# Optimization experiments

Measured on AMD Instinct MI355X. Metric: run time of the kernel, lower is better.

The kernel has to match this reference:

```python
import jax, jax.numpy as jnp
import numpy as np

V, H, B, T_ENC, S, T_DEC, G = 18000, 400, 16, 256, 30, 8, 3


def setup_inputs() -> dict:
    key = jax.random.key(0)
    ks = jax.random.split(key, 16)
    def n(k, shape, s=0.1):
        return jax.random.normal(k, shape, jnp.float32) * s
    return {
        'story': jax.random.randint(ks[0], (B, T_ENC), 0, V, dtype=jnp.int32),
        'target_batches': jax.random.randint(ks[1], (B, S, T_DEC), 0, V, dtype=jnp.int32),
        'emb': n(ks[2], (V, H)),
        'enc_Wih_f': n(ks[3], (3 * H, H)), 'enc_Whh_f': n(ks[4], (3 * H, H)),
        'enc_bih_f': jnp.zeros((3 * H,), jnp.float32), 'enc_bhh_f': jnp.zeros((3 * H,), jnp.float32),
        'enc_Wih_b': n(ks[5], (3 * H, H)), 'enc_Whh_b': n(ks[6], (3 * H, H)),
        'enc_bih_b': jnp.zeros((3 * H,), jnp.float32), 'enc_bhh_b': jnp.zeros((3 * H,), jnp.float32),
        'dec_Wih': n(ks[7], (3 * H, H)), 'dec_Whh': n(ks[8], (3 * H, H)),
        'dec_bih': jnp.zeros((3 * H,), jnp.float32), 'dec_bhh': jnp.zeros((3 * H,), jnp.float32),
        'W_ratio': n(ks[9], (1, 3 * H)), 'b_ratio': jnp.zeros((1,), jnp.float32),
        'W_gate': n(ks[10], (G, H)), 'b_gate': jnp.zeros((G,), jnp.float32),
        'slot_emb': n(ks[11], (S, H)),
    }


def _gru_step(h, x, Wih, Whh, bih, bhh):
    # PyTorch GRU gate order: r, z, n
    gi = x @ Wih.T + bih
    gh = h @ Whh.T + bhh
    ir, iz, ig = jnp.split(gi, 3, axis=-1)
    hr, hz, hg = jnp.split(gh, 3, axis=-1)
    r = jax.nn.sigmoid(ir + hr)
    z = jax.nn.sigmoid(iz + hz)
    g = jnp.tanh(ig + r * hg)
    return (1.0 - z) * g + z * h


def _run_gru(xs, h0, Wih, Whh, bih, bhh):
    def step(h, x):
        h2 = _gru_step(h, x, Wih, Whh, bih, bhh)
        return h2, h2
    hT, out = jax.lax.scan(step, h0, xs)
    return out, hT


def reference(story, target_batches, emb,
              enc_Wih_f, enc_Whh_f, enc_bih_f, enc_bhh_f,
              enc_Wih_b, enc_Whh_b, enc_bih_b, enc_bhh_b,
              dec_Wih, dec_Whh, dec_bih, dec_bhh,
              W_ratio, b_ratio, W_gate, b_gate, slot_emb):
    # ---- EncoderRNN (bidirectional 1-layer GRU; dropout=0 / eval mode) ----
    x = emb[story.T]                       # (T_enc, B, H)
    h0 = jnp.zeros((B, H), x.dtype)
    out_f, h_f = _run_gru(x, h0, enc_Wih_f, enc_Whh_f, enc_bih_f, enc_bhh_f)
    out_b_rev, h_b = _run_gru(x[::-1], h0, enc_Wih_b, enc_Whh_b, enc_bih_b, enc_bhh_b)
    out_b = out_b_rev[::-1]
    enc_out = jnp.transpose(out_f + out_b, (1, 0, 2))   # (B, T_enc, H) = fwd+bwd halves summed
    enc_hidden = h_f + h_b                               # (B, H)     = hidden[0] + hidden[1]

    # ---- Generator decode loop ----
    SB = S * B
    dec_in0 = jnp.broadcast_to(slot_emb[:, None, :], (S, B, H)).reshape(SB, H)
    h = jnp.tile(enc_hidden, (S, 1))                     # (SB, H)
    enc_tiled = jnp.tile(enc_out, (S, 1, 1))             # (SB, T_enc, H)
    story_tiled = jnp.tile(story, (S, 1))                # (SB, T_enc)
    rows = jnp.arange(SB)[:, None]
    # teacher-forcing tokens per step, slot-major flatten to (T_dec, SB)
    tf_tokens = jnp.transpose(target_batches, (2, 1, 0)).reshape(T_DEC, SB)

    def step(carry, tok):
        h, dec_in = carry
        h2 = _gru_step(h, dec_in, dec_Wih, dec_Whh, dec_bih, dec_bhh)  # dec_state == new hidden
        scores = jnp.einsum('nd,ntd->nt', h2, enc_tiled)               # attend (all lens == T_enc)
        prob = jax.nn.softmax(scores, axis=1)
        context = jnp.einsum('nt,ntd->nd', prob, enc_tiled)
        gate = context @ W_gate.T + b_gate                              # (SB, G)
        p_vocab = jax.nn.softmax(h2 @ emb.T, axis=1)                    # (SB, V)
        p_gen = jnp.concatenate([h2, context, dec_in], axis=-1)         # (SB, 3H)
        sw = jax.nn.sigmoid(p_gen @ W_ratio.T + b_ratio)                # (SB, 1)
        ptr = jnp.zeros((SB, V), prob.dtype).at[rows, story_tiled].add(prob)  # scatter_add copy dist
        final = (1.0 - sw) * ptr + sw * p_vocab
        dec_in_next = emb[tok]                                          # teacher forcing
        return (h2, dec_in_next), (final, gate)

    _, (finals, gates) = jax.lax.scan(step, (h, dec_in0), tf_tokens)
    all_pointer_outputs = finals.reshape(T_DEC, S, B, V).transpose(1, 2, 0, 3)  # (S, B, T_dec, V)
    all_gate_outputs = gates[0].reshape(S, B, G)                                 # gate from step 0
    return all_pointer_outputs, all_gate_outputs
```

## Files before the change

kernel.cpp:

```cpp
#include <hip/hip_runtime.h>
#include <cstdint>
#include <cstddef>

#define VV 18000
#define HH 400
#define H3 1200
#define H3P 1280
#define KP 416
#define BB 16
#define TE 256
#define SS 30
#define TDN 8
#define GGN 3
#define SBN 480
#define NROW_ENC 4096
#define VP 18048
#define MP_DEC 512

#define EBLK 25

typedef __bf16 bf16;
typedef __attribute__((ext_vector_type(8))) __bf16 bf16x8;
typedef __attribute__((ext_vector_type(4))) float f32x4;
typedef __attribute__((ext_vector_type(4))) unsigned int u32x4;

static __device__ __forceinline__ float sigf(float x) {
    return 1.0f / (1.0f + __expf(-x));
}

__global__ __launch_bounds__(256) void gemm_bt(const bf16* __restrict__ A,
                                               const bf16* __restrict__ B,
                                               float* __restrict__ C,
                                               int M, int N, int K) {
    __shared__ __align__(16) bf16 sA[128 * 32];
    __shared__ __align__(16) bf16 sB[128 * 32];
    const int tid = threadIdx.x;
    const int lane = tid & 63;
    const int wave = tid >> 6;
    const int wm = wave >> 1, wn = wave & 1;
    const int m0 = blockIdx.x * 128, n0 = blockIdx.y * 128;
    f32x4 acc[4][4] = {};
    const int c0 = tid, c1 = tid + 256;
    const int r0 = c0 >> 2, q0 = (c0 & 3) * 8;
    const int r1 = c1 >> 2, q1 = (c1 & 3) * 8;
    const int ar = lane & 15, ak = (lane >> 4) * 8;
    const int nk = K >> 5;
    for (int kt = 0; kt < nk; ++kt) {
        const int kb = kt * 32;
        uint4 a0 = *(const uint4*)(A + (size_t)(m0 + r0) * K + kb + q0);
        uint4 a1 = *(const uint4*)(A + (size_t)(m0 + r1) * K + kb + q1);
        uint4 b0 = *(const uint4*)(B + (size_t)(n0 + r0) * K + kb + q0);
        uint4 b1 = *(const uint4*)(B + (size_t)(n0 + r1) * K + kb + q1);
        __syncthreads();
        *(uint4*)(sA + r0 * 32 + q0) = a0;
        *(uint4*)(sA + r1 * 32 + q1) = a1;
        *(uint4*)(sB + r0 * 32 + q0) = b0;
        *(uint4*)(sB + r1 * 32 + q1) = b1;
        __syncthreads();
        bf16x8 af[4], bg[4];
#pragma unroll
        for (int i = 0; i < 4; ++i)
            af[i] = *(const bf16x8*)(sA + (wm * 64 + i * 16 + ar) * 32 + ak);
#pragma unroll
        for (int j = 0; j < 4; ++j)
            bg[j] = *(const bf16x8*)(sB + (wn * 64 + j * 16 + ar) * 32 + ak);
#pragma unroll
        for (int i = 0; i < 4; ++i)
#pragma unroll
            for (int j = 0; j < 4; ++j)
                acc[i][j] = __builtin_amdgcn_mfma_f32_16x16x32_bf16(af[i], bg[j], acc[i][j], 0, 0, 0);
    }
    const int cr = (lane >> 4) * 4, cc = lane & 15;
#pragma unroll
    for (int i = 0; i < 4; ++i)
#pragma unroll
        for (int j = 0; j < 4; ++j)
#pragma unroll
            for (int q = 0; q < 4; ++q) {
                int row = m0 + wm * 64 + i * 16 + cr + q;
                int col = n0 + wn * 64 + j * 16 + cc;
                C[(size_t)row * N + col] = acc[i][j][q];
            }
}

__global__ void prep_pad_bf16(const float* __restrict__ src, bf16* __restrict__ dst,
                              int rows_real, int cols_real, int rows_pad, int cols_pad) {
    int idx = blockIdx.x * blockDim.x + threadIdx.x;
    int total = rows_pad * cols_pad;
    if (idx >= total) return;
    int r = idx / cols_pad, c = idx % cols_pad;
    float v = (r < rows_real && c < cols_real) ? src[(size_t)r * cols_real + c] : 0.f;
    dst[idx] = (bf16)v;
}

__global__ void prep_aenc(const int* __restrict__ story, const float* __restrict__ emb,
                          bf16* __restrict__ dst) {
    int idx = blockIdx.x * blockDim.x + threadIdx.x;
    if (idx >= NROW_ENC * KP) return;
    int m = idx / KP, k = idx % KP;
    int t = m >> 4, b = m & 15;
    float v = 0.f;
    if (k < HH) {
        int tok = story[b * TE + t];
        v = emb[(size_t)tok * HH + k];
    }
    dst[idx] = (bf16)v;
}

__global__ void prep_decx(const int* __restrict__ target, const float* __restrict__ emb,
                          const float* __restrict__ slot, float* __restrict__ xf,
                          bf16* __restrict__ xb) {
    int idx = blockIdx.x * blockDim.x + threadIdx.x;
    if (idx >= TDN * SBN * KP) return;
    int k = idx % KP;
    int nn = idx / KP;
    int n = nn % SBN;
    int td = nn / SBN;
    int s = n >> 4, b = n & 15;
    float v = 0.f;
    if (k < HH) {
        if (td == 0) v = slot[s * HH + k];
        else {
            int tok = target[(b * SS + s) * TDN + (td - 1)];
            v = emb[(size_t)tok * HH + k];
        }
        xf[((size_t)td * SBN + n) * HH + k] = v;
    }
    xb[idx] = (bf16)v;
}

__global__ void zero_bf16k(bf16* dst, int total) {
    int idx = blockIdx.x * blockDim.x + threadIdx.x;
    if (idx < total) dst[idx] = (bf16)0.f;
}

__global__ __launch_bounds__(256) void enc_rnn10(
    const float* __restrict__ gi_f, const float* __restrict__ gi_b,
    const float* __restrict__ whh_f, const float* __restrict__ whh_b,
    const float* __restrict__ bih_f, const float* __restrict__ bhh_f,
    const float* __restrict__ bih_b, const float* __restrict__ bhh_b,
    float* __restrict__ hist_f, float* __restrict__ hist_b,
    unsigned int* __restrict__ hbuf_f, unsigned int* __restrict__ hbuf_b,
    unsigned int* __restrict__ flags) {
    const int dir = blockIdx.x & 1;
    const int blk = blockIdx.x >> 1;
    const int j0 = blk * 16;
    const float* gi  = dir ? gi_b : gi_f;
    const float* whh = dir ? whh_b : whh_f;
    const float* bih = dir ? bih_b : bih_f;
    const float* bhh = dir ? bhh_b : bhh_f;
    float* hist = dir ? hist_b : hist_f;
    unsigned int* hbuf = dir ? hbuf_b : hbuf_f;

    __shared__ float GHL[3 * 256];

    const int tid = threadIdx.x;
    const int wv = tid >> 6, lane = tid & 63;

    const int ub = tid >> 4, ucol = tid & 15;
    const int uj = j0 + ucol;
    const float bihr = bih[uj], bihz = bih[HH + uj], bihg = bih[2 * HH + uj];
    const float bhhr = bhh[uj], bhhz = bhh[HH + uj], bhhg = bhh[2 * HH + uj];

    const int kk0 = (lane >> 4) * 8;
    bf16x8 Bf[13];
    if (wv < 3) {
        const int brow = wv * HH + j0 + (lane & 15);
#pragma unroll
        for (int ks = 0; ks < 13; ++ks) {
            bf16x8 v;
#pragma unroll
            for (int e = 0; e < 8; ++e) {
                int k = kk0 + ks * 32 + e;
                v[e] = (k < HH) ? (bf16)whh[(size_t)brow * HH + k] : (bf16)0.f;
            }
            Bf[ks] = v;
        }
    }

    union UV { unsigned int d[4]; bf16x8 v; };

    float hp = 0.f;

    for (int s = 0; s < TE; ++s) {
        const int tt = dir ? (TE - 1 - s) : s;
        const float* gir = gi + ((size_t)tt * BB + ub) * H3P;
        float gi0 = gir[uj];
        float gi1 = gir[HH + uj];
        float gi2 = gir[2 * HH + uj];

        f32x4 acc0 = {}, acc1 = {};
        if (s > 0) {
            if (wv == 0) {
                const unsigned int* fl = flags + ((size_t)dir * TE + (s - 1)) * 32;
                while (true) {
                    unsigned f = 1u;
                    if (lane < EBLK)
                        asm volatile("global_load_dword %0, %1, off sc0 sc1"
                                     : "=v"(f) : "v"(fl + lane));
                    asm volatile("s_waitcnt vmcnt(0)" ::: "memory");
                    if (__all((int)(f != 0u))) break;
                }
            }
            __syncthreads();
            if (wv < 3) {
                const int ttp = dir ? (tt + 1) : (tt - 1);
                const unsigned int* hrow =
                    hbuf + ((size_t)ttp * BB + (lane & 15)) * KP + kk0;
                u32x4 ua[13], ubv[13];
#pragma unroll
                for (int ks = 0; ks < 13; ++ks) {
                    asm volatile("global_load_dwordx4 %0, %1, off offset:%c2 sc0 sc1"
                                 : "=v"(ua[ks]) : "v"(hrow), "n"(ks * 128));
                    asm volatile("global_load_dwordx4 %0, %1, off offset:%c2 sc0 sc1"
                                 : "=v"(ubv[ks]) : "v"(hrow), "n"(ks * 128 + 16));
                }
                asm volatile("s_waitcnt vmcnt(0)" ::: "memory");
                __builtin_amdgcn_sched_barrier(0);
#pragma unroll
                for (int ks = 0; ks < 13; ++ks) {
                    u32x4 a = ua[ks], b = ubv[ks];
                    UV ah, al;
                    ah.d[0] = (a.x & 0xffffu) | (a.y << 16);
                    ah.d[1] = (a.z & 0xffffu) | (a.w << 16);
                    ah.d[2] = (b.x & 0xffffu) | (b.y << 16);
                    ah.d[3] = (b.z & 0xffffu) | (b.w << 16);
                    al.d[0] = (a.x >> 16) | (a.y & 0xffff0000u);
                    al.d[1] = (a.z >> 16) | (a.w & 0xffff0000u);
                    al.d[2] = (b.x >> 16) | (b.y & 0xffff0000u);
                    al.d[3] = (b.z >> 16) | (b.w & 0xffff0000u);
                    acc0 = __builtin_amdgcn_mfma_f32_16x16x32_bf16(ah.v, Bf[ks], acc0, 0, 0, 0);
                    acc1 = __builtin_amdgcn_mfma_f32_16x16x32_bf16(al.v, Bf[ks], acc1, 0, 0, 0);
                }
            }
        }
        if (wv < 3) {
            f32x4 at = acc0 + acc1;
            const int cb0 = wv * 256 + ((lane >> 4) * 4) * 16 + (lane & 15);
            GHL[cb0]      = at[0];
            GHL[cb0 + 16] = at[1];
            GHL[cb0 + 32] = at[2];
            GHL[cb0 + 48] = at[3];
        }
        __syncthreads();

        float ghr = GHL[tid];
        float ghz = GHL[256 + tid];
        float ghg = GHL[512 + tid];
        float r = sigf(gi0 + bihr + ghr + bhhr);
        float z = sigf(gi1 + bihz + ghz + bhhz);
        float g = tanhf(gi2 + bihg + r * (ghg + bhhg));
        float hn = (1.f - z) * g + z * hp;
        hp = hn;
        hist[((size_t)tt * BB + ub) * HH + uj] = hn;
        bf16 hi = (bf16)hn;
        bf16 lo = (bf16)(hn - (float)hi);
        unsigned int pk = (unsigned int)__builtin_bit_cast(unsigned short, hi)
                        | ((unsigned int)__builtin_bit_cast(unsigned short, lo) << 16);
        unsigned int* hw = hbuf + ((size_t)tt * BB + ub) * KP + uj;
        asm volatile("global_store_dword %0, %1, off sc0 sc1" :: "v"(hw), "v"(pk) : "memory");

        asm volatile("s_waitcnt vmcnt(0)" ::: "memory");
        __syncthreads();
        if (tid == 0) {
            unsigned int one = 1u;
            unsigned int* fw = flags + ((size_t)dir * TE + s) * 32 + blk;
            asm volatile("global_store_dword %0, %1, off sc0 sc1" :: "v"(fw), "v"(one) : "memory");
        }
    }
}

__global__ void combine_enc(const float* __restrict__ hf, const float* __restrict__ hb,
                            float* __restrict__ enc_out) {
    int idx = blockIdx.x * blockDim.x + threadIdx.x;
    if (idx >= BB * TE * HH) return;
    int hcol = idx % HH;
    int t = (idx / HH) % TE;
    int b = idx / (HH * TE);
    size_t src = ((size_t)t * BB + b) * HH + hcol;
    enc_out[idx] = hf[src] + hb[src];
}

__global__ void init_hdec2(const float* __restrict__ hf, const float* __restrict__ hb,
                           float* __restrict__ hdec, bf16* __restrict__ h2b) {
    int idx = blockIdx.x * blockDim.x + threadIdx.x;
    if (idx >= SBN * HH) return;
    int hcol = idx % HH;
    int n = idx / HH;
    int b = n & 15;
    float v = hf[((size_t)(TE - 1) * BB + b) * HH + hcol] + hb[((size_t)b) * HH + hcol];
    hdec[idx] = v;
    h2b[(size_t)n * KP + hcol] = (bf16)v;
}

__global__ void gru_dec2(const float* __restrict__ gi, const float* __restrict__ gh,
                         const float* __restrict__ bih, const float* __restrict__ bhh,
                         const float* __restrict__ hprev, float* __restrict__ hnew,
                         bf16* __restrict__ h2b) {
    int idx = blockIdx.x * blockDim.x + threadIdx.x;
    if (idx >= SBN * HH) return;
    int n = idx / HH, j = idx % HH;
    const float* gir = gi + (size_t)n * H3P;
    const float* ghr = gh + (size_t)n * H3P;
    float r = sigf(gir[j] + bih[j] + ghr[j] + bhh[j]);
    float z = sigf(gir[HH + j] + bih[HH + j] + ghr[HH + j] + bhh[HH + j]);
    float g = tanhf(gir[2 * HH + j] + bih[2 * HH + j] + r * (ghr[2 * HH + j] + bhh[2 * HH + j]));
    float hn = (1.f - z) * g + z * hprev[idx];
    hnew[idx] = hn;
    h2b[(size_t)n * KP + j] = (bf16)hn;
}

__global__ __launch_bounds__(256) void attn2(const float* __restrict__ h2,
                                             const float* __restrict__ enc,
                                             const float* __restrict__ dx,
                                             const float* __restrict__ Wr, const float* __restrict__ br,
                                             const float* __restrict__ Wg, const float* __restrict__ bg,
                                             float* __restrict__ prob,
                                             float* __restrict__ sw, float* __restrict__ outg,
                                             int isfirst) {
    int n = blockIdx.x, b = n & 15, tid = threadIdx.x;
    __shared__ __align__(16) float hq[HH];
    __shared__ __align__(16) float cx[HH];
    __shared__ float sc[TE];
    __shared__ float red[4];
    for (int k = tid; k < HH; k += 256) hq[k] = h2[(size_t)n * HH + k];
    __syncthreads();
    const float4* er = (const float4*)(enc + ((size_t)b * TE + tid) * HH);
    const float4* hq4 = (const float4*)hq;
    float acc = 0.f;
#pragma unroll 4
    for (int k = 0; k < HH / 4; ++k) {
        float4 e = er[k];
        float4 hv = hq4[k];
        acc += e.x * hv.x + e.y * hv.y + e.z * hv.z + e.w * hv.w;
    }
    float m = acc;
    for (int d = 32; d; d >>= 1) m = fmaxf(m, __shfl_xor(m, d));
    if ((tid & 63) == 0) red[tid >> 6] = m;
    __syncthreads();
    m = fmaxf(fmaxf(red[0], red[1]), fmaxf(red[2], red[3]));
    __syncthreads();
    float e = __expf(acc - m);
    float ssum = e;
    for (int d = 32; d; d >>= 1) ssum += __shfl_xor(ssum, d);
    if ((tid & 63) == 0) red[tid >> 6] = ssum;
    __syncthreads();
    ssum = red[0] + red[1] + red[2] + red[3];
    float p = e / ssum;
    sc[tid] = p;
    prob[(size_t)n * TE + tid] = p;
    __syncthreads();
    for (int hcol = tid; hcol < HH; hcol += 256) {
        float a = 0.f;
        for (int t = 0; t < TE; ++t) a += sc[t] * enc[((size_t)b * TE + t) * HH + hcol];
        cx[hcol] = a;
    }
    __syncthreads();
    float a = 0.f;
    for (int k = tid; k < H3; k += 256) {
        float v = (k < HH) ? hq[k]
                : (k < 2 * HH) ? cx[k - HH]
                : dx[(size_t)n * HH + (k - 2 * HH)];
        a += v * Wr[k];
    }
    for (int d = 32; d; d >>= 1) a += __shfl_xor(a, d);
    if ((tid & 63) == 0) red[tid >> 6] = a;
    __syncthreads();
    if (tid == 0) sw[n] = sigf(red[0] + red[1] + red[2] + red[3] + br[0]);
    if (isfirst) {
#pragma unroll
        for (int g = 0; g < GGN; ++g) {
            float b2 = 0.f;
            for (int k = tid; k < HH; k += 256) b2 += cx[k] * Wg[g * HH + k];
            for (int d = 32; d; d >>= 1) b2 += __shfl_xor(b2, d);
            __syncthreads();
            if ((tid & 63) == 0) red[tid >> 6] = b2;
            __syncthreads();
            if (tid == 0) outg[n * GGN + g] = red[0] + red[1] + red[2] + red[3] + bg[g];
        }
    }
}

__global__ __launch_bounds__(1024) void smax_final(const float* __restrict__ logits,
                                                   const float* __restrict__ sw,
                                                   float* __restrict__ out, int td) {
    int n = blockIdx.x, tid = threadIdx.x;
    __shared__ float red[16];
    __shared__ float bc[2];
    float v[18];
    float mx = -1e30f;
#pragma unroll
    for (int i = 0; i < 18; ++i) {
        int c = tid + (i << 10);
        v[i] = (c < VV) ? logits[(size_t)n * VP + c] : -1e30f;
        mx = fmaxf(mx, v[i]);
    }
    for (int d = 32; d; d >>= 1) mx = fmaxf(mx, __shfl_xor(mx, d));
    if ((tid & 63) == 0) red[tid >> 6] = mx;
    __syncthreads();
    if (tid == 0) {
        float m2 = red[0];
        for (int w = 1; w < 16; ++w) m2 = fmaxf(m2, red[w]);
        bc[0] = m2;
    }
    __syncthreads();
    mx = bc[0];
    float s = 0.f;
#pragma unroll
    for (int i = 0; i < 18; ++i) {
        int c = tid + (i << 10);
        if (c < VV) { v[i] = __expf(v[i] - mx); s += v[i]; }
    }
    for (int d = 32; d; d >>= 1) s += __shfl_xor(s, d);
    if ((tid & 63) == 0) red[tid >> 6] = s;
    __syncthreads();
    if (tid == 0) {
        float s2 = 0.f;
        for (int w = 0; w < 16; ++w) s2 += red[w];
        bc[1] = s2;
    }
    __syncthreads();
    float scale = sw[n] / bc[1];
    float* orow = out + ((size_t)n * TDN + td) * VV;
#pragma unroll
    for (int i = 0; i < 18; ++i) {
        int c = tid + (i << 10);
        if (c < VV) orow[c] = v[i] * scale;
    }
}

__global__ void scatter_ptr(const int* __restrict__ story, const float* __restrict__ prob,
                            const float* __restrict__ sw, float* __restrict__ out, int td) {
    int n = blockIdx.x, t = threadIdx.x, b = n & 15;
    int tok = story[b * TE + t];
    float val = (1.f - sw[n]) * prob[(size_t)n * TE + t];
    atomicAdd(out + ((size_t)n * TDN + td) * VV + tok, val);
}

static inline int cdiv(long long a, long long b) { return (int)((a + b - 1) / b); }

extern "C" void kernel_launch(void* const* d_in, const int* in_sizes, int n_in,
                              void* d_out, int out_size, void* d_ws, size_t ws_size,
                              hipStream_t stream) {
    const int*   story  = (const int*)d_in[0];
    const int*   target = (const int*)d_in[1];
    const float* emb    = (const float*)d_in[2];
    const float* wih_f  = (const float*)d_in[3];
    const float* whh_f  = (const float*)d_in[4];
    const float* bih_f  = (const float*)d_in[5];
    const float* bhh_f  = (const float*)d_in[6];
    const float* wih_b  = (const float*)d_in[7];
    const float* whh_b  = (const float*)d_in[8];
    const float* bih_b  = (const float*)d_in[9];
    const float* bhh_b  = (const float*)d_in[10];
    const float* dwih   = (const float*)d_in[11];
    const float* dwhh   = (const float*)d_in[12];
    const float* dbih   = (const float*)d_in[13];
    const float* dbhh   = (const float*)d_in[14];
    const float* wr     = (const float*)d_in[15];
    const float* brr    = (const float*)d_in[16];
    const float* wgg    = (const float*)d_in[17];
    const float* bgg    = (const float*)d_in[18];
    const float* slot   = (const float*)d_in[19];
    float* out = (float*)d_out;

    char* wsb = (char*)d_ws;
    size_t off = 0;
    auto alloc = [&](size_t bytes) -> char* {
        char* p = wsb + off;
        off = (off + bytes + 255) & ~(size_t)255;
        return p;
    };
    bf16*  embb  = (bf16*)alloc((size_t)VP * KP * 2);
    bf16*  aenc  = (bf16*)alloc((size_t)NROW_ENC * KP * 2);
    bf16*  wfb   = (bf16*)alloc((size_t)H3P * KP * 2);
    bf16*  wbb   = (bf16*)alloc((size_t)H3P * KP * 2);
    bf16*  dwihb = (bf16*)alloc((size_t)H3P * KP * 2);
    bf16*  dwhhb = (bf16*)alloc((size_t)H3P * KP * 2);
    bf16*  decxb = (bf16*)alloc((size_t)TDN * SBN * KP * 2);
    bf16*  h2b   = (bf16*)alloc((size_t)MP_DEC * KP * 2);
    unsigned int* hbuff = (unsigned int*)alloc((size_t)TE * BB * KP * 4);
    unsigned int* hbufb = (unsigned int*)alloc((size_t)TE * BB * KP * 4);
    unsigned int* flags = (unsigned int*)alloc((size_t)2 * TE * 32 * 4);
    float* gif   = (float*)alloc((size_t)NROW_ENC * H3P * 4);
    float* gib   = (float*)alloc((size_t)NROW_ENC * H3P * 4);
    float* gidec = (float*)alloc((size_t)TDN * SBN * H3P * 4);
    float* ghdec = (float*)alloc((size_t)MP_DEC * H3P * 4);
    float* histf = (float*)alloc((size_t)TE * BB * HH * 4);
    float* histb = (float*)alloc((size_t)TE * BB * HH * 4);
    float* encout= (float*)alloc((size_t)BB * TE * HH * 4);
    float* decxf = (float*)alloc((size_t)TDN * SBN * HH * 4);
    float* hA    = (float*)alloc((size_t)SBN * HH * 4);
    float* hB    = (float*)alloc((size_t)SBN * HH * 4);
    float* probw = (float*)alloc((size_t)SBN * TE * 4);
    float* sww   = (float*)alloc((size_t)SBN * 4);
    float* logits= (float*)alloc((size_t)MP_DEC * VP * 4);
    (void)ws_size; (void)in_sizes; (void)n_in; (void)out_size;

    (void)hipMemsetAsync(flags, 0, (size_t)2 * TE * 32 * 4, stream);

    const int thr = 256;
    prep_pad_bf16<<<cdiv((long long)VP * KP, thr), thr, 0, stream>>>(emb, embb, VV, HH, VP, KP);
    prep_aenc<<<cdiv((long long)NROW_ENC * KP, thr), thr, 0, stream>>>(story, emb, aenc);
    prep_pad_bf16<<<cdiv((long long)H3P * KP, thr), thr, 0, stream>>>(wih_f, wfb, H3, HH, H3P, KP);
    prep_pad_bf16<<<cdiv((long long)H3P * KP, thr), thr, 0, stream>>>(wih_b, wbb, H3, HH, H3P, KP);
    prep_pad_bf16<<<cdiv((long long)H3P * KP, thr), thr, 0, stream>>>(dwih, dwihb, H3, HH, H3P, KP);
    prep_pad_bf16<<<cdiv((long long)H3P * KP, thr), thr, 0, stream>>>(dwhh, dwhhb, H3, HH, H3P, KP);
    prep_decx<<<cdiv((long long)TDN * SBN * KP, thr), thr, 0, stream>>>(target, emb, slot, decxf, decxb);
    zero_bf16k<<<cdiv((long long)MP_DEC * KP, thr), thr, 0, stream>>>(h2b, MP_DEC * KP);

    {
        dim3 g(NROW_ENC / 128, H3P / 128);
        gemm_bt<<<g, 256, 0, stream>>>(aenc, wfb, gif, NROW_ENC, H3P, KP);
        gemm_bt<<<g, 256, 0, stream>>>(aenc, wbb, gib, NROW_ENC, H3P, KP);
    }
    {
        dim3 g((TDN * SBN) / 128, H3P / 128);
        gemm_bt<<<g, 256, 0, stream>>>(decxb, dwihb, gidec, TDN * SBN, H3P, KP);
    }

    enc_rnn10<<<2 * EBLK, 256, 0, stream>>>(gif, gib, whh_f, whh_b,
                                            bih_f, bhh_f, bih_b, bhh_b,
                                            histf, histb, hbuff, hbufb, flags);

    combine_enc<<<cdiv((long long)BB * TE * HH, thr), thr, 0, stream>>>(histf, histb, encout);
    init_hdec2<<<cdiv((long long)SBN * HH, thr), thr, 0, stream>>>(histf, histb, hA, h2b);

    float* hc = hA;
    float* hn = hB;
    for (int td = 0; td < TDN; ++td) {
        {
            dim3 g(MP_DEC / 128, H3P / 128);
            gemm_bt<<<g, 256, 0, stream>>>(h2b, dwhhb, ghdec, MP_DEC, H3P, KP);
        }
        gru_dec2<<<cdiv((long long)SBN * HH, thr), thr, 0, stream>>>(
            gidec + (size_t)td * SBN * H3P, ghdec, dbih, dbhh, hc, hn, h2b);
        attn2<<<SBN, 256, 0, stream>>>(hn, encout, decxf + (size_t)td * SBN * HH,
                                       wr, brr, wgg, bgg, probw, sww,
                                       out + (size_t)SBN * TDN * VV, td == 0 ? 1 : 0);
        {
            dim3 g(MP_DEC / 128, VP / 128);
            gemm_bt<<<g, 256, 0, stream>>>(h2b, embb, logits, MP_DEC, VP, KP);
        }
        smax_final<<<SBN, 1024, 0, stream>>>(logits, sww, out, td);
        scatter_ptr<<<SBN, TE, 0, stream>>>(story, probw, sww, out, td);
        float* tmp = hc; hc = hn; hn = tmp;
    }
}
```

Before: 1.957 ms.

## Hoist attention out of decoder loop, batch slots per block, fuse scatter into softmax

```diff
diff --git a/kernel.cpp b/kernel.cpp
--- a/kernel.cpp
+++ b/kernel.cpp
@@ -129,8 +129,8 @@
     xb[idx] = (bf16)v;
 }
 
-__global__ void zero_bf16k(bf16* dst, int total) {
-    int idx = blockIdx.x * blockDim.x + threadIdx.x;
+__global__ void zero_bf16k(bf16* dst, size_t total) {
+    size_t idx = (size_t)blockIdx.x * blockDim.x + threadIdx.x;
     if (idx < total) dst[idx] = (bf16)0.f;
 }
 
@@ -310,80 +310,134 @@
     h2b[(size_t)n * KP + j] = (bf16)hn;
 }
 
-__global__ __launch_bounds__(256) void attn2(const float* __restrict__ h2,
-                                             const float* __restrict__ enc,
-                                             const float* __restrict__ dx,
-                                             const float* __restrict__ Wr, const float* __restrict__ br,
-                                             const float* __restrict__ Wg, const float* __restrict__ bg,
-                                             float* __restrict__ prob,
-                                             float* __restrict__ sw, float* __restrict__ outg,
-                                             int isfirst) {
-    int n = blockIdx.x, b = n & 15, tid = threadIdx.x;
-    __shared__ __align__(16) float hq[HH];
-    __shared__ __align__(16) float cx[HH];
-    __shared__ float sc[TE];
-    __shared__ float red[4];
-    for (int k = tid; k < HH; k += 256) hq[k] = h2[(size_t)n * HH + k];
-    __syncthreads();
-    const float4* er = (const float4*)(enc + ((size_t)b * TE + tid) * HH);
-    const float4* hq4 = (const float4*)hq;
-    float acc = 0.f;
-#pragma unroll 4
-    for (int k = 0; k < HH / 4; ++k) {
-        float4 e = er[k];
-        float4 hv = hq4[k];
-        acc += e.x * hv.x + e.y * hv.y + e.z * hv.z + e.w * hv.w;
-    }
-    float m = acc;
-    for (int d = 32; d; d >>= 1) m = fmaxf(m, __shfl_xor(m, d));
-    if ((tid & 63) == 0) red[tid >> 6] = m;
-    __syncthreads();
-    m = fmaxf(fmaxf(red[0], red[1]), fmaxf(red[2], red[3]));
-    __syncthreads();
-    float e = __expf(acc - m);
-    float ssum = e;
-    for (int d = 32; d; d >>= 1) ssum += __shfl_xor(ssum, d);
-    if ((tid & 63) == 0) red[tid >> 6] = ssum;
-    __syncthreads();
-    ssum = red[0] + red[1] + red[2] + red[3];
-    float p = e / ssum;
-    sc[tid] = p;
-    prob[(size_t)n * TE + tid] = p;
-    __syncthreads();
-    for (int hcol = tid; hcol < HH; hcol += 256) {
+__global__ __launch_bounds__(256) void attn3(
+    const float* __restrict__ hfall,
+    const float* __restrict__ enc,
+    const float* __restrict__ decxf,
+    const float* __restrict__ Wr, const float* __restrict__ br,
+    const float* __restrict__ Wg, const float* __restrict__ bg,
+    float* __restrict__ probw,
+    float* __restrict__ sww,
+    float* __restrict__ outg) {
+    const int b = blockIdx.x >> 1;
+    const int half = blockIdx.x & 1;
+    const int td = blockIdx.y;
+    const int s0 = half * 15;
+    const int tid = threadIdx.x;
+    const int lane = tid & 63, wv = tid >> 6;
+
+    __shared__ __align__(16) float h2L[15][HH];
+    __shared__ __align__(16) float scL[15][TE];
+    __shared__ __align__(16) float cxL[15][HH];
+
+    const float* h2base = hfall + (size_t)(td + 1) * SBN * HH;
+    for (int i = tid; i < 15 * HH; i += 256) {
+        int j = i / HH, k = i % HH;
+        int n = (s0 + j) * BB + b;
+        h2L[j][k] = h2base[(size_t)n * HH + k];
+    }
+    __syncthreads();
+
+    {
+        float acc[15];
+#pragma unroll
+        for (int j = 0; j < 15; ++j) acc[j] = 0.f;
+        const float4* er = (const float4*)(enc + ((size_t)b * TE + tid) * HH);
+        for (int k4 = 0; k4 < HH / 4; ++k4) {
+            float4 e = er[k4];
+#pragma unroll
+            for (int j = 0; j < 15; ++j) {
+                float4 hv = *(const float4*)(&h2L[j][k4 * 4]);
+                acc[j] += e.x * hv.x + e.y * hv.y + e.z * hv.z + e.w * hv.w;
+            }
+        }
+#pragma unroll
+        for (int j = 0; j < 15; ++j) scL[j][tid] = acc[j];
+    }
+    __syncthreads();
+
+    for (int j = wv; j < 15; j += 4) {
+        float v0 = scL[j][lane], v1 = scL[j][lane + 64];
+        float v2 = scL[j][lane + 128], v3 = scL[j][lane + 192];
+        float m = fmaxf(fmaxf(v0, v1), fmaxf(v2, v3));
+        for (int d = 32; d; d >>= 1) m = fmaxf(m, __shfl_xor(m, d));
+        v0 = __expf(v0 - m); v1 = __expf(v1 - m);
+        v2 = __expf(v2 - m); v3 = __expf(v3 - m);
+        float s = v0 + v1 + v2 + v3;
+        for (int d = 32; d; d >>= 1) s += __shfl_xor(s, d);
+        float inv = 1.f / s;
+        scL[j][lane]       = v0 * inv;
+        scL[j][lane + 64]  = v1 * inv;
+        scL[j][lane + 128] = v2 * inv;
+        scL[j][lane + 192] = v3 * inv;
+    }
+    __syncthreads();
+
+    for (int i = tid; i < 15 * TE; i += 256) {
+        int j = i / TE, t = i % TE;
+        int n = (s0 + j) * BB + b;
+        probw[((size_t)td * SBN + n) * TE + t] = scL[j][t];
+    }
+
+    {
+        float cx0[15], cx1[15];
+#pragma unroll
+        for (int j = 0; j < 15; ++j) { cx0[j] = 0.f; cx1[j] = 0.f; }
+        const int c0 = tid, c1 = tid + 256;
+        const bool has2 = (c1 < HH);
+        for (int t = 0; t < TE; t += 2) {
+            const float* e0r = enc + ((size_t)b * TE + t) * HH;
+            const float* e1r = e0r + HH;
+            float e00 = e0r[c0], e01 = e1r[c0];
+            float e10 = 0.f, e11 = 0.f;
+            if (has2) { e10 = e0r[c1]; e11 = e1r[c1]; }
+#pragma unroll
+            for (int j = 0; j < 15; ++j) {
+                float2 p = *(const float2*)(&scL[j][t]);
+                cx0[j] += p.x * e00 + p.y * e01;
+                cx1[j] += p.x * e10 + p.y * e11;
+            }
+        }
+#pragma unroll
+        for (int j = 0; j < 15; ++j) {
+            cxL[j][c0] = cx0[j];
+            if (has2) cxL[j][c1] = cx1[j];
+        }
+    }
+    __syncthreads();
+
+    for (int j = wv; j < 15; j += 4) {
+        int n = (s0 + j) * BB + b;
+        const float* dx = decxf + ((size_t)td * SBN + n) * HH;
         float a = 0.f;
-        for (int t = 0; t < TE; ++t) a += sc[t] * enc[((size_t)b * TE + t) * HH + hcol];
-        cx[hcol] = a;
-    }
-    __syncthreads();
-    float a = 0.f;
-    for (int k = tid; k < H3; k += 256) {
-        float v = (k < HH) ? hq[k]
-                : (k < 2 * HH) ? cx[k - HH]
-                : dx[(size_t)n * HH + (k - 2 * HH)];
-        a += v * Wr[k];
-    }
-    for (int d = 32; d; d >>= 1) a += __shfl_xor(a, d);
-    if ((tid & 63) == 0) red[tid >> 6] = a;
-    __syncthreads();
-    if (tid == 0) sw[n] = sigf(red[0] + red[1] + red[2] + red[3] + br[0]);
-    if (isfirst) {
-#pragma unroll
-        for (int g = 0; g < GGN; ++g) {
-            float b2 = 0.f;
-            for (int k = tid; k < HH; k += 256) b2 += cx[k] * Wg[g * HH + k];
-            for (int d = 32; d; d >>= 1) b2 += __shfl_xor(b2, d);
-            __syncthreads();
-            if ((tid & 63) == 0) red[tid >> 6] = b2;
-            __syncthreads();
-            if (tid == 0) outg[n * GGN + g] = red[0] + red[1] + red[2] + red[3] + bg[g];
-        }
-    }
-}
-
-__global__ __launch_bounds__(1024) void smax_final(const float* __restrict__ logits,
-                                                   const float* __restrict__ sw,
-                                                   float* __restrict__ out, int td) {
+        for (int k = lane; k < H3; k += 64) {
+            float v = (k < HH) ? h2L[j][k]
+                    : (k < 2 * HH) ? cxL[j][k - HH]
+                    : dx[k - 2 * HH];
+            a += v * Wr[k];
+        }
+        for (int d = 32; d; d >>= 1) a += __shfl_xor(a, d);
+        if (lane == 0) sww[(size_t)td * SBN + n] = sigf(a + br[0]);
+    }
+
+    if (td == 0) {
+        for (int j = wv; j < 15; j += 4) {
+            int n = (s0 + j) * BB + b;
+#pragma unroll
+            for (int g = 0; g < GGN; ++g) {
+                float a = 0.f;
+                for (int k = lane; k < HH; k += 64) a += cxL[j][k] * Wg[g * HH + k];
+                for (int d = 32; d; d >>= 1) a += __shfl_xor(a, d);
+                if (lane == 0) outg[n * GGN + g] = a + bg[g];
+            }
+        }
+    }
+}
+
+__global__ __launch_bounds__(1024) void smax_scatter(
+    const float* __restrict__ logits, const float* __restrict__ sw,
+    const int* __restrict__ story, const float* __restrict__ probtd,
+    float* __restrict__ out, int td) {
     int n = blockIdx.x, tid = threadIdx.x;
     __shared__ float red[16];
     __shared__ float bc[2];
@@ -420,21 +474,21 @@
         bc[1] = s2;
     }
     __syncthreads();
-    float scale = sw[n] / bc[1];
+    float swv = sw[n];
+    float scale = swv / bc[1];
     float* orow = out + ((size_t)n * TDN + td) * VV;
 #pragma unroll
     for (int i = 0; i < 18; ++i) {
         int c = tid + (i << 10);
         if (c < VV) orow[c] = v[i] * scale;
     }
-}
-
-__global__ void scatter_ptr(const int* __restrict__ story, const float* __restrict__ prob,
-                            const float* __restrict__ sw, float* __restrict__ out, int td) {
-    int n = blockIdx.x, t = threadIdx.x, b = n & 15;
-    int tok = story[b * TE + t];
-    float val = (1.f - sw[n]) * prob[(size_t)n * TE + t];
-    atomicAdd(out + ((size_t)n * TDN + td) * VV + tok, val);
+    __syncthreads();
+    if (tid < TE) {
+        int b = n & 15;
+        int tok = story[b * TE + tid];
+        float val = (1.f - swv) * probtd[(size_t)n * TE + tid];
+        atomicAdd(orow + tok, val);
+    }
 }
 
 static inline int cdiv(long long a, long long b) { return (int)((a + b - 1) / b); }
@@ -478,7 +532,7 @@
     bf16*  dwihb = (bf16*)alloc((size_t)H3P * KP * 2);
     bf16*  dwhhb = (bf16*)alloc((size_t)H3P * KP * 2);
     bf16*  decxb = (bf16*)alloc((size_t)TDN * SBN * KP * 2);
-    bf16*  h2b   = (bf16*)alloc((size_t)MP_DEC * KP * 2);
+    bf16*  h2ball= (bf16*)alloc((size_t)9 * MP_DEC * KP * 2);
     unsigned int* hbuff = (unsigned int*)alloc((size_t)TE * BB * KP * 4);
     unsigned int* hbufb = (unsigned int*)alloc((size_t)TE * BB * KP * 4);
     unsigned int* flags = (unsigned int*)alloc((size_t)2 * TE * 32 * 4);
@@ -490,10 +544,9 @@
     float* histb = (float*)alloc((size_t)TE * BB * HH * 4);
     float* encout= (float*)alloc((size_t)BB * TE * HH * 4);
     float* decxf = (float*)alloc((size_t)TDN * SBN * HH * 4);
-    float* hA    = (float*)alloc((size_t)SBN * HH * 4);
-    float* hB    = (float*)alloc((size_t)SBN * HH * 4);
-    float* probw = (float*)alloc((size_t)SBN * TE * 4);
-    float* sww   = (float*)alloc((size_t)SBN * 4);
+    float* hfall = (float*)alloc((size_t)9 * SBN * HH * 4);
+    float* probw = (float*)alloc((size_t)TDN * SBN * TE * 4);
+    float* sww   = (float*)alloc((size_t)TDN * SBN * 4);
     float* logits= (float*)alloc((size_t)MP_DEC * VP * 4);
     (void)ws_size; (void)in_sizes; (void)n_in; (void)out_size;
 
@@ -507,7 +560,7 @@
     prep_pad_bf16<<<cdiv((long long)H3P * KP, thr), thr, 0, stream>>>(dwih, dwihb, H3, HH, H3P, KP);
     prep_pad_bf16<<<cdiv((long long)H3P * KP, thr), thr, 0, stream>>>(dwhh, dwhhb, H3, HH, H3P, KP);
     prep_decx<<<cdiv((long long)TDN * SBN * KP, thr), thr, 0, stream>>>(target, emb, slot, decxf, decxb);
-    zero_bf16k<<<cdiv((long long)MP_DEC * KP, thr), thr, 0, stream>>>(h2b, MP_DEC * KP);
+    zero_bf16k<<<cdiv((long long)9 * MP_DEC * KP, thr), thr, 0, stream>>>(h2ball, (size_t)9 * MP_DEC * KP);
 
     {
         dim3 g(NROW_ENC / 128, H3P / 128);
@@ -524,26 +577,30 @@
                                             histf, histb, hbuff, hbufb, flags);
 
     combine_enc<<<cdiv((long long)BB * TE * HH, thr), thr, 0, stream>>>(histf, histb, encout);
-    init_hdec2<<<cdiv((long long)SBN * HH, thr), thr, 0, stream>>>(histf, histb, hA, h2b);
-
-    float* hc = hA;
-    float* hn = hB;
+    init_hdec2<<<cdiv((long long)SBN * HH, thr), thr, 0, stream>>>(histf, histb, hfall, h2ball);
+
     for (int td = 0; td < TDN; ++td) {
-        {
-            dim3 g(MP_DEC / 128, H3P / 128);
-            gemm_bt<<<g, 256, 0, stream>>>(h2b, dwhhb, ghdec, MP_DEC, H3P, KP);
-        }
+        dim3 g(MP_DEC / 128, H3P / 128);
+        gemm_bt<<<g, 256, 0, stream>>>(h2ball + (size_t)td * MP_DEC * KP, dwhhb, ghdec,
+                                       MP_DEC, H3P, KP);
         gru_dec2<<<cdiv((long long)SBN * HH, thr), thr, 0, stream>>>(
-            gidec + (size_t)td * SBN * H3P, ghdec, dbih, dbhh, hc, hn, h2b);
-        attn2<<<SBN, 256, 0, stream>>>(hn, encout, decxf + (size_t)td * SBN * HH,
-                                       wr, brr, wgg, bgg, probw, sww,
-                                       out + (size_t)SBN * TDN * VV, td == 0 ? 1 : 0);
-        {
-            dim3 g(MP_DEC / 128, VP / 128);
-            gemm_bt<<<g, 256, 0, stream>>>(h2b, embb, logits, MP_DEC, VP, KP);
-        }
-        smax_final<<<SBN, 1024, 0, stream>>>(logits, sww, out, td);
-        scatter_ptr<<<SBN, TE, 0, stream>>>(story, probw, sww, out, td);
-        float* tmp = hc; hc = hn; hn = tmp;
-    }
-}
+            gidec + (size_t)td * SBN * H3P, ghdec, dbih, dbhh,
+            hfall + (size_t)td * SBN * HH,
+            hfall + (size_t)(td + 1) * SBN * HH,
+            h2ball + (size_t)(td + 1) * MP_DEC * KP);
+    }
+
+    {
+        dim3 g(32, TDN);
+        attn3<<<g, 256, 0, stream>>>(hfall, encout, decxf, wr, brr, wgg, bgg,
+                                     probw, sww, out + (size_t)SBN * TDN * VV);
+    }
+
+    for (int td = 0; td < TDN; ++td) {
+        dim3 g(MP_DEC / 128, VP / 128);
+        gemm_bt<<<g, 256, 0, stream>>>(h2ball + (size_t)(td + 1) * MP_DEC * KP, embb, logits,
+                                       MP_DEC, VP, KP);
+        smax_scatter<<<SBN, 1024, 0, stream>>>(logits, sww + (size_t)td * SBN, story,
+                                               probw + (size_t)td * SBN * TE, out, td);
+    }
+}
```

Result: faster. 1.870 ms (-4.4%).
